# Kernel optimization log

Measured on AMD Instinct MI355X. Metric: run time of the kernel, lower is better.

## Reference

```python
import jax, jax.numpy as jnp
import numpy as np
from math import log2, ceil

HEADS = 16
BLOCK = 16
EPS = 1e-8


def flip_every_two(t):
    # flip adjacent pairs along axis 1: (B, n, ...) with n even
    B, n = t.shape[0], t.shape[1]
    rest = t.shape[2:]
    t = t.reshape(B, n // 2, 2, *rest)
    t = jnp.flip(t, axis=2)
    return t.reshape(B, n, *rest)


def masked_aggregate(t, mask, average=True):
    # t: (B, n, 2, d), mask: (B, n, 2) bool; aggregate over axis=2
    m = mask[..., None]
    s = jnp.where(m, t, 0.0).sum(axis=2)
    total = mask.sum(axis=2)  # (B, n) int
    if average:
        s = s / jnp.clip(total, 1)[..., None].astype(t.dtype)
    return jnp.where((total == 0)[..., None], 0.0, s)


def _forward(x, Wq, bq, Wk, bk, Wv, bv, mask):
    b, n, hidden = x.shape
    h, bsz, d = HEADS, BLOCK, hidden // HEADS
    scale = d ** -0.5
    pad_to_len = 2 ** ceil(log2(n))
    pad = pad_to_len - n
    if pad != 0:
        x = jnp.pad(x, ((0, 0), (0, pad), (0, 0)))
        mask = jnp.pad(mask, ((0, 0), (0, pad)), constant_values=False)
    N = pad_to_len

    def split_heads(t):  # (b, N, h*d) -> (b*h, N, d)
        return t.reshape(b, N, h, d).transpose(0, 2, 1, 3).reshape(b * h, N, d)

    q = split_heads(x @ Wq + bq) * scale
    k = split_heads(x @ Wk + bk)
    v = split_heads(x @ Wv + bv)
    m = jnp.broadcast_to(mask[:, None, :], (b, h, N)).reshape(b * h, N)

    num_levels = int(log2(N // bsz)) - 2
    qkvs = [(q, k, v, m)]
    for _ in range(num_levels):
        B, L, _ = q.shape
        q2 = q.reshape(B, L // 2, 2, d)
        k2 = k.reshape(B, L // 2, 2, d)
        v2 = v.reshape(B, L // 2, 2, d)
        m2 = m.reshape(B, L // 2, 2)
        q = masked_aggregate(q2, m2, average=True)
        k = masked_aggregate(k2, m2, average=True)
        v = masked_aggregate(v2, m2, average=False)
        m = jnp.any(m2, axis=2)
        qkvs.append((q, k, v, m))
    qkvs = [qkvs[0]] + qkvs

    Ys = []
    for ind, (ql, kl, vl, ml) in enumerate(reversed(qkvs)):
        is_last = ind == len(qkvs) - 1
        B, L, _ = ql.shape
        nb = L // bsz
        qb = ql.reshape(B, nb, bsz, d)
        kb = kl.reshape(B, nb, bsz, d)
        vb = vl.reshape(B, nb, bsz, d)
        mb = ml.reshape(B, nb, bsz)
        k_mask = mb if is_last else flip_every_two(mb)
        S_mask = mb[..., :, None] & k_mask[..., None, :]  # (B, nb, bsz, bsz)
        if not is_last:
            kb = flip_every_two(kb)
            vb = flip_every_two(vb)
        S = jnp.einsum('bnid,bnjd->bnij', qb, kb)
        S = jnp.where(S_mask, S, jnp.finfo(S.dtype).min)
        S = S - S.max(axis=-1, keepdims=True)
        A = jnp.exp(S)
        Y = jnp.einsum('bnij,bnjd->bnid', A, vb)
        Ys.append((Y.reshape(B, L, d), A.sum(axis=-1).reshape(B, L)))

    Y, A = Ys[0]
    for ind in range(1, len(Ys)):
        is_last = ind == len(Ys) - 1
        if not is_last:
            Y = jnp.repeat(Y, 2, axis=1)
            A = jnp.repeat(A, 2, axis=1)
        Y = Ys[ind][0] + Y
        A = Ys[ind][1] + A

    out = Y / (A + EPS)[..., None]  # (b*h, N, d)
    out = out.reshape(b, h, N, d).transpose(0, 2, 1, 3).reshape(b, N, hidden)
    return out[:, :n]


def setup_inputs():
    key = jax.random.key(0)
    ks = jax.random.split(key, 7)
    b, n, hidden = 2, 8192, 1024
    s = 1.0 / np.sqrt(hidden)
    x = jax.random.normal(ks[0], (b, n, hidden), jnp.float32)
    mask = jnp.ones((b, n), dtype=bool)
    Wq = jax.random.normal(ks[1], (hidden, hidden), jnp.float32) * s
    Wk = jax.random.normal(ks[2], (hidden, hidden), jnp.float32) * s
    Wv = jax.random.normal(ks[3], (hidden, hidden), jnp.float32) * s
    bq = jax.random.normal(ks[4], (hidden,), jnp.float32) * 0.01
    bk = jax.random.normal(ks[5], (hidden,), jnp.float32) * 0.01
    bv = jax.random.normal(ks[6], (hidden,), jnp.float32) * 0.01
    return {"x": x, "mask": mask, "Wq": Wq, "bq": bq, "Wk": Wk, "bk": bk, "Wv": Wv, "bv": bv}


def reference(x, mask, Wq, bq, Wk, bk, Wv, bv):
    return _forward(x, Wq, bq, Wk, bk, Wv, bv, mask)
```

## Files before the change

kernel.cpp:

```cpp
#include <hip/hip_runtime.h>
#include <hip/hip_bf16.h>

typedef __attribute__((ext_vector_type(4))) float f32x4;
typedef __attribute__((ext_vector_type(8))) __bf16 bf16x8;
typedef __attribute__((ext_vector_type(4))) unsigned int u32x4;

#define TE 33423360ull

__device__ __forceinline__ unsigned short f2b_rne(float f) {
  unsigned u = __float_as_uint(f);
  return (unsigned short)((u + 0x7fffu + ((u >> 16) & 1u)) >> 16);
}
__device__ __forceinline__ float b2f(unsigned s) { return __uint_as_float(s << 16); }

__device__ __forceinline__ void gload_lds16(const unsigned short* g, unsigned short* l) {
  __builtin_amdgcn_global_load_lds((const __attribute__((address_space(1))) void*)g,
                                   (__attribute__((address_space(3))) void*)l, 16, 0, 0);
}

__global__ void conv_x(const float* __restrict__ x, unsigned short* __restrict__ xb) {
  size_t i = ((size_t)blockIdx.x * 256 + threadIdx.x) * 8;
  f32x4 A = *(const f32x4*)(x + i);
  f32x4 B = *(const f32x4*)(x + i + 4);
  u32x4 o;
  o[0] = f2b_rne(A[0]) | ((unsigned)f2b_rne(A[1]) << 16);
  o[1] = f2b_rne(A[2]) | ((unsigned)f2b_rne(A[3]) << 16);
  o[2] = f2b_rne(B[0]) | ((unsigned)f2b_rne(B[1]) << 16);
  o[3] = f2b_rne(B[2]) | ((unsigned)f2b_rne(B[3]) << 16);
  *(u32x4*)(xb + i) = o;
}

__global__ void transpose_w(const float* __restrict__ Wq, const float* __restrict__ Wk,
                            const float* __restrict__ Wv, unsigned short* __restrict__ wt) {
  int z = blockIdx.z;
  const float* W = (z == 0) ? Wq : (z == 1) ? Wk : Wv;
  __shared__ float t[32][33];
  int n0 = blockIdx.x * 32, k0 = blockIdx.y * 32;
  int tx = threadIdx.x, ty = threadIdx.y;
#pragma unroll
  for (int j = 0; j < 4; ++j)
    t[ty + j * 8][tx] = W[(size_t)(k0 + ty + j * 8) * 1024 + n0 + tx];
  __syncthreads();
  unsigned short* o = wt + (size_t)z * 1048576;
#pragma unroll
  for (int j = 0; j < 4; ++j)
    o[(size_t)(n0 + ty + j * 8) * 1024 + k0 + tx] = f2b_rne(t[tx][ty + j * 8]);
}

__global__ __launch_bounds__(256, 2) void gemm_qkv(
    const unsigned short* __restrict__ xb, const unsigned short* __restrict__ wt,
    const float* __restrict__ bq, const float* __restrict__ bk, const float* __restrict__ bv,
    unsigned short* __restrict__ qkv) {
  int flat = blockIdx.y * 8 + blockIdx.x;
  int swz = (flat & 7) * 128 + (flat >> 3);
  int m0 = (swz >> 3) * 128, n0 = (swz & 7) * 128;
  __shared__ unsigned short lds[32768];
  int tid = threadIdx.x;
  int lane = tid & 63, wid = tid >> 6;
  int g = lane >> 4, r16 = lane & 15;
  int wm = (wid >> 1) * 64, wn = (wid & 1) * 64;
  int srow = wid * 16 + (lane >> 2);
  int sc8 = ((lane & 3) ^ ((lane >> 3) & 3)) * 8;

  auto stage = [&](int b, int kt) {
    unsigned short* Tb = lds + b * 16384;
    int kc = kt * 32 + sc8;
#pragma unroll
    for (int a = 0; a < 2; ++a) {
      gload_lds16(xb + (size_t)(m0 + a * 64 + srow) * 1024 + kc, Tb + a * 2048 + wid * 512);
#pragma unroll
      for (int z = 0; z < 3; ++z)
        gload_lds16(wt + (size_t)z * 1048576 + (size_t)(n0 + a * 64 + srow) * 1024 + kc,
                    Tb + 4096 + z * 4096 + a * 2048 + wid * 512);
    }
  };

  f32x4 acc[3][4][4];
#pragma unroll
  for (int z = 0; z < 3; ++z)
#pragma unroll
    for (int i = 0; i < 4; ++i)
#pragma unroll
      for (int j = 0; j < 4; ++j) acc[z][i][j] = (f32x4){0.f, 0.f, 0.f, 0.f};

  int slot8 = (g ^ ((r16 >> 1) & 3)) * 8;

  stage(0, 0);
  stage(1, 1);
  for (int kt = 0; kt < 32; ++kt) {
    int cb = kt & 1;
    if (kt < 31) asm volatile("s_waitcnt vmcnt(8)" ::: "memory");
    else         asm volatile("s_waitcnt vmcnt(0)" ::: "memory");
    __builtin_amdgcn_s_barrier();
    __builtin_amdgcn_sched_barrier(0);
    const unsigned short* Tb = lds + cb * 16384;
    bf16x8 af[4];
#pragma unroll
    for (int t = 0; t < 4; ++t)
      af[t] = *(const bf16x8*)(Tb + (wm + t * 16 + r16) * 32 + slot8);
#pragma unroll
    for (int z = 0; z < 3; ++z) {
      bf16x8 bf_[4];
#pragma unroll
      for (int t = 0; t < 4; ++t)
        bf_[t] = *(const bf16x8*)(Tb + 4096 + z * 4096 + (wn + t * 16 + r16) * 32 + slot8);
#pragma unroll
      for (int i = 0; i < 4; ++i)
#pragma unroll
        for (int j = 0; j < 4; ++j)
          acc[z][i][j] = __builtin_amdgcn_mfma_f32_16x16x32_bf16(af[i], bf_[j], acc[z][i][j], 0, 0, 0);
    }
    __builtin_amdgcn_sched_barrier(0);
    __builtin_amdgcn_s_barrier();
    if (kt < 30) stage(cb, kt + 2);
  }

  unsigned short* Ct = lds;
#pragma unroll
  for (int z = 0; z < 3; ++z) {
    const float* bias = (z == 0) ? bq : (z == 1) ? bk : bv;
    float scale = (z == 0) ? 0.125f : 1.0f;
#pragma unroll
    for (int pass = 0; pass < 2; ++pass) {
      __syncthreads();
      if ((wid >> 1) == pass) {
#pragma unroll
        for (int i = 0; i < 4; ++i) {
#pragma unroll
          for (int j = 0; j < 4; ++j) {
            int col = wn + j * 16 + r16;
            float bc = bias[n0 + col];
#pragma unroll
            for (int r = 0; r < 4; ++r) {
              int rl = i * 16 + g * 4 + r;
              Ct[rl * 144 + col] = f2b_rne((acc[z][i][j][r] + bc) * scale);
            }
          }
        }
      }
      __syncthreads();
      int rl = tid >> 2, q = tid & 3;
      int R = m0 + pass * 64 + rl;
      int colg = n0 + q * 32;
      int bh = ((R >> 13) << 4) + (colg >> 6);
      unsigned short* op =
          qkv + (size_t)z * TE + ((size_t)bh * 8192 + (size_t)(R & 8191)) * 64 + (q & 1) * 32;
#pragma unroll
      for (int ch = 0; ch < 4; ++ch)
        *(u32x4*)(op + ch * 8) = *(const u32x4*)(Ct + rl * 144 + q * 32 + ch * 8);
    }
  }
}

__global__ __launch_bounds__(256) void agg_all(unsigned short* __restrict__ qkv) {
  int seg = blockIdx.x, bh = blockIdx.y, z = blockIdx.z;
  unsigned short* tb = qkv + (size_t)z * TE;
  __shared__ unsigned short b0[16384];
  __shared__ unsigned short b1[8192];
  int t = threadIdx.x;
  const unsigned short* ip = tb + ((size_t)bh * 8192 + (size_t)seg * 256) * 64;
#pragma unroll
  for (int j = 0; j < 8; ++j)
    *(u32x4*)(b0 + (j * 256 + t) * 8) = *(const u32x4*)(ip + (size_t)(j * 256 + t) * 8);
  __syncthreads();
  float sc = (z < 2) ? 0.5f : 1.0f;
  long off = 8192;
  unsigned short* src = b0;
  unsigned short* dst = b1;
  for (int l = 1; l <= 7; ++l) {
    int R = 256 >> l;
    int chunks = R * 32;
    for (int c = t; c < chunks; c += 256) {
      int r = c >> 5, cc = c & 31;
      unsigned a = *(const unsigned*)(src + (2 * r) * 64 + cc * 2);
      unsigned b = *(const unsigned*)(src + (2 * r + 1) * 64 + cc * 2);
      float lo = (b2f(a & 0xffffu) + b2f(b & 0xffffu)) * sc;
      float hi = (b2f(a >> 16) + b2f(b >> 16)) * sc;
      unsigned o = f2b_rne(lo) | ((unsigned)f2b_rne(hi) << 16);
      *(unsigned*)(dst + r * 64 + cc * 2) = o;
      unsigned short* op =
          tb + (size_t)off * 2048 + ((size_t)bh * (8192 >> l) + (size_t)seg * R + r) * 64;
      *(unsigned*)(op + cc * 2) = o;
    }
    __syncthreads();
    off += 8192 >> l;
    unsigned short* tmp = src; src = dst; dst = tmp;
  }
}

union U8 { bf16x8 v; unsigned short u[8]; };

__device__ __forceinline__ void attn_unit(
    const unsigned short* kb, const unsigned short* vb, bf16x8 qf0, bf16x8 qf1,
    int g, int qr, f32x4 (&acc)[4], float& aacc) {
  bf16x8 kf0 = *(const bf16x8*)(kb + qr * 64 + g * 8);
  bf16x8 kf1 = *(const bf16x8*)(kb + qr * 64 + 32 + g * 8);
  f32x4 s = {0.f, 0.f, 0.f, 0.f};
  s = __builtin_amdgcn_mfma_f32_16x16x32_bf16(kf0, qf0, s, 0, 0, 0);
  s = __builtin_amdgcn_mfma_f32_16x16x32_bf16(kf1, qf1, s, 0, 0, 0);
  float mx = fmaxf(fmaxf(s[0], s[1]), fmaxf(s[2], s[3]));
  mx = fmaxf(mx, __shfl_xor(mx, 16));
  mx = fmaxf(mx, __shfl_xor(mx, 32));
  float av[4], asum = 0.f;
#pragma unroll
  for (int r = 0; r < 4; ++r) { av[r] = __expf(s[r] - mx); asum += av[r]; }
  asum += __shfl_xor(asum, 16);
  asum += __shfl_xor(asum, 32);
  aacc += asum;
  U8 A_;
#pragma unroll
  for (int r = 0; r < 4; ++r) A_.u[r] = f2b_rne(av[r]);
#pragma unroll
  for (int r = 4; r < 8; ++r) A_.u[r] = 0;
#pragma unroll
  for (int cg = 0; cg < 4; ++cg) {
    int c = cg * 16 + qr;
    U8 B_;
#pragma unroll
    for (int r = 0; r < 4; ++r) B_.u[r] = vb[(g * 4 + r) * 64 + c];
#pragma unroll
    for (int r = 4; r < 8; ++r) B_.u[r] = 0;
    acc[cg] = __builtin_amdgcn_mfma_f32_16x16x32_bf16(A_.v, B_.v, acc[cg], 0, 0, 0);
  }
}

__global__ __launch_bounds__(256) void attn_fused(const unsigned short* __restrict__ qkv,
                                                  float* __restrict__ outp) {
  int flat = blockIdx.y * 512 + blockIdx.x;
  int swz = (flat & 7) * 512 + (flat >> 3);
  int fb = swz * 4 + (threadIdx.x >> 6);
  int bh = fb >> 9, B0 = fb & 511;
  int lane = threadIdx.x & 63;
  int g = lane >> 4, qr = lane & 15;
  const unsigned short* qt = qkv;
  const unsigned short* kt = qkv + TE;
  const unsigned short* vt = qkv + 2 * TE;
  f32x4 acc[4];
#pragma unroll
  for (int cg = 0; cg < 4; ++cg) acc[cg] = (f32x4){0.f, 0.f, 0.f, 0.f};
  float aacc = 0.f;
  int off = 0;
#pragma unroll
  for (int l = 0; l <= 7; ++l) {
    int L = 8192 >> l;
    size_t base = (size_t)off * 2048 + (size_t)bh * L * 64;
    const unsigned short* qb = qt + base;
    const unsigned short* kb = kt + base;
    const unsigned short* vb = vt + base;
    int qrow = (B0 * 16 + qr) >> l;
    bf16x8 qf0 = *(const bf16x8*)(qb + (size_t)qrow * 64 + g * 8);
    bf16x8 qf1 = *(const bf16x8*)(qb + (size_t)qrow * 64 + 32 + g * 8);
    int P = B0 >> l;
    if (l == 0) {
      attn_unit(kb + (size_t)P * 1024, vb + (size_t)P * 1024, qf0, qf1, g, qr, acc, aacc);
      attn_unit(kb + (size_t)(P ^ 1) * 1024, vb + (size_t)(P ^ 1) * 1024, qf0, qf1, g, qr, acc, aacc);
    } else {
      int S_ = P ^ 1;
      attn_unit(kb + (size_t)S_ * 1024, vb + (size_t)S_ * 1024, qf0, qf1, g, qr, acc, aacc);
    }
    off += L;
  }
  int b_ = bh >> 4, h_ = bh & 15;
#pragma unroll
  for (int r = 0; r < 4; ++r) {
    int p = g * 4 + r;
    float ap = __shfl(aacc, p);
    float inv = 1.0f / (ap + 1e-8f);
    float* od = outp + ((size_t)(b_ * 8192 + B0 * 16 + p)) * 1024 + h_ * 64 + qr;
#pragma unroll
    for (int cg = 0; cg < 4; ++cg) od[cg * 16] = acc[cg][r] * inv;
  }
}

extern "C" void kernel_launch(void* const* d_in, const int* in_sizes, int n_in,
                              void* d_out, int out_size, void* d_ws, size_t ws_size,
                              hipStream_t stream) {
  const float* x = (const float*)d_in[0];
  const float* Wq = (const float*)d_in[2];
  const float* bq = (const float*)d_in[3];
  const float* Wk = (const float*)d_in[4];
  const float* bk = (const float*)d_in[5];
  const float* Wv = (const float*)d_in[6];
  const float* bv = (const float*)d_in[7];
  float* out = (float*)d_out;

  char* ws = (char*)d_ws;
  size_t o = 0;
  unsigned short* qkv = (unsigned short*)(ws + o); o += 200540160ull;
  unsigned short* wt = (unsigned short*)(ws + o); o += 6291456ull;
  unsigned short* xb = (unsigned short*)(ws + o); o += 33554432ull;
  if (ws_size < o) return;

  conv_x<<<8192, 256, 0, stream>>>(x, xb);
  transpose_w<<<dim3(32, 32, 3), dim3(32, 8), 0, stream>>>(Wq, Wk, Wv, wt);
  gemm_qkv<<<dim3(8, 128), 256, 0, stream>>>(xb, wt, bq, bk, bv, qkv);
  agg_all<<<dim3(32, 32, 3), 256, 0, stream>>>(qkv);
  attn_fused<<<dim3(512, 8), 256, 0, stream>>>(qkv, out);
}
```

Before: 243.0 us.

## Fuse hierarchical pair-aggregation into QKV GEMM epilogue, drop agg_all kernel

The QKV GEMM epilogue now writes the whole 128x128 output tile into LDS at once, stores the level-0 rows, and then builds all seven coarser aggregation levels from LDS, writing each to global memory. This removes the separate agg_all launch, which re-read the full Q/K/V tensors from global memory. In exchange the GEMM epilogue becomes longer and uses more LDS (extra ping-pong buffers), which could reduce occupancy. Each block's aggregation now works on 128-row segments instead of 256, so more global stores are narrow 4-byte writes.

```diff
diff --git a/kernel.cpp b/kernel.cpp
--- a/kernel.cpp
+++ b/kernel.cpp
@@ -116,75 +116,62 @@
   }
 
   unsigned short* Ct = lds;
+  unsigned short* bufA = lds + 17408;
+  unsigned short* bufB = lds + 26112;
+  int bh0 = ((m0 >> 13) << 4) + (n0 >> 6);
+  int pos0 = m0 & 8191;
 #pragma unroll
   for (int z = 0; z < 3; ++z) {
     const float* bias = (z == 0) ? bq : (z == 1) ? bk : bv;
     float scale = (z == 0) ? 0.125f : 1.0f;
-#pragma unroll
-    for (int pass = 0; pass < 2; ++pass) {
-      __syncthreads();
-      if ((wid >> 1) == pass) {
-#pragma unroll
-        for (int i = 0; i < 4; ++i) {
-#pragma unroll
-          for (int j = 0; j < 4; ++j) {
-            int col = wn + j * 16 + r16;
-            float bc = bias[n0 + col];
-#pragma unroll
-            for (int r = 0; r < 4; ++r) {
-              int rl = i * 16 + g * 4 + r;
-              Ct[rl * 144 + col] = f2b_rne((acc[z][i][j][r] + bc) * scale);
-            }
-          }
-        }
+    float asc = (z < 2) ? 0.5f : 1.0f;
+    unsigned short* tbz = qkv + (size_t)z * TE;
+    __syncthreads();
+#pragma unroll
+    for (int i = 0; i < 4; ++i) {
+#pragma unroll
+      for (int j = 0; j < 4; ++j) {
+        int col = wn + j * 16 + r16;
+        float bc = bias[n0 + col];
+#pragma unroll
+        for (int r = 0; r < 4; ++r)
+          Ct[(wm + i * 16 + g * 4 + r) * 136 + col] = f2b_rne((acc[z][i][j][r] + bc) * scale);
+      }
+    }
+    __syncthreads();
+    {
+      int rl = tid >> 1, half = tid & 1;
+      unsigned short* op = tbz + ((size_t)(bh0 + half) * 8192 + pos0 + rl) * 64;
+#pragma unroll
+      for (int ch = 0; ch < 8; ++ch)
+        *(u32x4*)(op + ch * 8) = *(const u32x4*)(Ct + rl * 136 + half * 64 + ch * 8);
+    }
+    unsigned short* src = Ct;
+    long off = 8192;
+    int Lc = 128;
+    for (int l = 1; l <= 7; ++l) {
+      int R = Lc >> 1;
+      unsigned short* dst = (l & 1) ? bufA : bufB;
+      int items = R * 64;
+      int Lp = 8192 >> l;
+      for (int c = tid; c < items; c += 256) {
+        int r = c >> 6, c2 = c & 63;
+        unsigned a = *(const unsigned*)(src + (2 * r) * 136 + c2 * 2);
+        unsigned b = *(const unsigned*)(src + (2 * r + 1) * 136 + c2 * 2);
+        float lo = (b2f(a & 0xffffu) + b2f(b & 0xffffu)) * asc;
+        float hi = (b2f(a >> 16) + b2f(b >> 16)) * asc;
+        unsigned o = f2b_rne(lo) | ((unsigned)f2b_rne(hi) << 16);
+        *(unsigned*)(dst + r * 136 + c2 * 2) = o;
+        int hp = c2 >> 5;
+        unsigned short* op = tbz + (size_t)off * 2048 +
+            ((size_t)(bh0 + hp) * Lp + (pos0 >> l) + r) * 64 + (c2 & 31) * 2;
+        *(unsigned*)op = o;
       }
       __syncthreads();
-      int rl = tid >> 2, q = tid & 3;
-      int R = m0 + pass * 64 + rl;
-      int colg = n0 + q * 32;
-      int bh = ((R >> 13) << 4) + (colg >> 6);
-      unsigned short* op =
-          qkv + (size_t)z * TE + ((size_t)bh * 8192 + (size_t)(R & 8191)) * 64 + (q & 1) * 32;
-#pragma unroll
-      for (int ch = 0; ch < 4; ++ch)
-        *(u32x4*)(op + ch * 8) = *(const u32x4*)(Ct + rl * 144 + q * 32 + ch * 8);
-    }
-  }
-}
-
-__global__ __launch_bounds__(256) void agg_all(unsigned short* __restrict__ qkv) {
-  int seg = blockIdx.x, bh = blockIdx.y, z = blockIdx.z;
-  unsigned short* tb = qkv + (size_t)z * TE;
-  __shared__ unsigned short b0[16384];
-  __shared__ unsigned short b1[8192];
-  int t = threadIdx.x;
-  const unsigned short* ip = tb + ((size_t)bh * 8192 + (size_t)seg * 256) * 64;
-#pragma unroll
-  for (int j = 0; j < 8; ++j)
-    *(u32x4*)(b0 + (j * 256 + t) * 8) = *(const u32x4*)(ip + (size_t)(j * 256 + t) * 8);
-  __syncthreads();
-  float sc = (z < 2) ? 0.5f : 1.0f;
-  long off = 8192;
-  unsigned short* src = b0;
-  unsigned short* dst = b1;
-  for (int l = 1; l <= 7; ++l) {
-    int R = 256 >> l;
-    int chunks = R * 32;
-    for (int c = t; c < chunks; c += 256) {
-      int r = c >> 5, cc = c & 31;
-      unsigned a = *(const unsigned*)(src + (2 * r) * 64 + cc * 2);
-      unsigned b = *(const unsigned*)(src + (2 * r + 1) * 64 + cc * 2);
-      float lo = (b2f(a & 0xffffu) + b2f(b & 0xffffu)) * sc;
-      float hi = (b2f(a >> 16) + b2f(b >> 16)) * sc;
-      unsigned o = f2b_rne(lo) | ((unsigned)f2b_rne(hi) << 16);
-      *(unsigned*)(dst + r * 64 + cc * 2) = o;
-      unsigned short* op =
-          tb + (size_t)off * 2048 + ((size_t)bh * (8192 >> l) + (size_t)seg * R + r) * 64;
-      *(unsigned*)(op + cc * 2) = o;
-    }
-    __syncthreads();
-    off += 8192 >> l;
-    unsigned short* tmp = src; src = dst; dst = tmp;
+      off += Lp;
+      Lc = R;
+      src = dst;
+    }
   }
 }
 
@@ -294,6 +281,5 @@
   conv_x<<<8192, 256, 0, stream>>>(x, xb);
   transpose_w<<<dim3(32, 32, 3), dim3(32, 8), 0, stream>>>(Wq, Wk, Wv, wt);
   gemm_qkv<<<dim3(8, 128), 256, 0, stream>>>(xb, wt, bq, bk, bv, qkv);
-  agg_all<<<dim3(32, 32, 3), 256, 0, stream>>>(qkv);
   attn_fused<<<dim3(512, 8), 256, 0, stream>>>(qkv, out);
 }
```

New measurement: 232.2 us. -4.4%, faster.
